# Kernel tuning notes

Hardware: AMD Instinct MI355X
Metric: run time of the kernel (lower is better)

The kernel has to match this reference:

```python
import jax, jax.numpy as jnp
import numpy as np

B, C, Np, D = 16, 64, 128, 128
HT = 4      # time heads
HS = 4      # space heads (GAT)
F = D       # GAT out_channels
DK = D // 2 # q/k proj dim
TOPK = 8
NEG = -1e30

def ln(x, g, b):
    m = x.mean(-1, keepdims=True)
    v = jnp.mean((x - m) ** 2, axis=-1, keepdims=True)
    return (x - m) / jnp.sqrt(v + 1e-5) * g + b

def setup_inputs() -> dict:
    key = jax.random.key(0)
    ks = jax.random.split(key, 16)
    w = lambda k, s: (jax.random.normal(k, s, jnp.float32) * 0.02)
    return dict(
        H_in=jax.random.normal(ks[0], (B, C, Np, D), jnp.float32),
        static_adj=jax.random.normal(ks[1], (C, C), jnp.float32) * 0.1,
        attn_in_w=w(ks[2], (3 * D, D)), attn_in_b=jnp.zeros((3 * D,), jnp.float32),
        attn_out_w=w(ks[3], (D, D)), attn_out_b=jnp.zeros((D,), jnp.float32),
        ln1_g=jnp.ones((D,), jnp.float32), ln1_b=jnp.zeros((D,), jnp.float32),
        ln2_g=jnp.ones((D,), jnp.float32), ln2_b=jnp.zeros((D,), jnp.float32),
        ff1_w=w(ks[4], (4 * D, D)), ff1_b=jnp.zeros((4 * D,), jnp.float32),
        ff2_w=w(ks[5], (D, 4 * D)), ff2_b=jnp.zeros((D,), jnp.float32),
        tnorm_g=jnp.ones((D,), jnp.float32), tnorm_b=jnp.zeros((D,), jnp.float32),
        q_w=w(ks[6], (DK, D)), q_b=jnp.zeros((DK,), jnp.float32),
        k_w=w(ks[7], (DK, D)), k_b=jnp.zeros((DK,), jnp.float32),
        gat_w=w(ks[8], (HS, F, D)),
        gat_att_src=w(ks[9], (HS, F)), gat_att_dst=w(ks[10], (HS, F)),
        gat_bias=jnp.zeros((D,), jnp.float32),
        snorm_g=jnp.ones((D,), jnp.float32), snorm_b=jnp.zeros((D,), jnp.float32),
    )

def _forward(H_in, static_adj, attn_in_w, attn_in_b, attn_out_w, attn_out_b,
             ln1_g, ln1_b, ln2_g, ln2_b, ff1_w, ff1_b, ff2_w, ff2_b,
             tnorm_g, tnorm_b, q_w, q_b, k_w, k_b,
             gat_w, gat_att_src, gat_att_dst, gat_bias, snorm_g, snorm_b):
    dh = D // HT
    # ---- temporal transformer encoder layer (norm_first) on [B*C, Np, D]
    x0 = H_in.reshape(B * C, Np, D)
    h = ln(x0, ln1_g, ln1_b)
    qkv = h @ attn_in_w.T + attn_in_b
    q, k, v = jnp.split(qkv, 3, axis=-1)
    q = q.reshape(-1, Np, HT, dh).transpose(0, 2, 1, 3)
    k = k.reshape(-1, Np, HT, dh).transpose(0, 2, 1, 3)
    v = v.reshape(-1, Np, HT, dh).transpose(0, 2, 1, 3)
    att = jax.nn.softmax(jnp.einsum('nhqd,nhkd->nhqk', q, k) / jnp.sqrt(jnp.float32(dh)), axis=-1)
    o = jnp.einsum('nhqk,nhkd->nhqd', att, v).transpose(0, 2, 1, 3).reshape(-1, Np, D)
    x = x0 + (o @ attn_out_w.T + attn_out_b)
    h2 = ln(x, ln2_g, ln2_b)
    x = x + jax.nn.relu(h2 @ ff1_w.T + ff1_b) @ ff2_w.T + ff2_b
    H_temp = ln(x0 + x, tnorm_g, tnorm_b).reshape(B, C, Np, D)
    # ---- dynamic adjacency from temporal summary
    Hs = H_temp.mean(axis=2)                              # [B,C,D]
    q2 = Hs @ q_w.T + q_b
    k2 = Hs @ k_w.T + k_b
    sim = jnp.einsum('bcd,bed->bce', q2, k2) * (DK ** -0.5)
    A = jnp.tanh(sim) + static_adj[None]                  # [B,C,C]
    # ---- top-k edge mask per sample (row r -> its top-k cols, no self loops)
    kk = max(1, min(TOPK, C - 1))
    idx = jax.lax.top_k(A, kk)[1]                         # [B,C,kk]
    mask = jnp.any(jax.nn.one_hot(idx, C, dtype=bool), axis=2)  # [B,C,C]
    mask = mask & (~jnp.eye(C, dtype=bool)) & (A != 0)
    # ---- dense masked GAT over all (B, Np) graphs; src=row, dst=col
    xh = jnp.einsum('bcpd,hfd->bphcf', H_temp, gat_w)     # [B,Np,HS,C,F]
    asrc = jnp.einsum('bphcf,hf->bphc', xh, gat_att_src)
    adst = jnp.einsum('bphcf,hf->bphc', xh, gat_att_dst)
    e = asrc[..., :, None] + adst[..., None, :]           # [B,Np,HS,src,dst]
    e = jnp.where(e > 0, e, 0.2 * e)                      # LeakyReLU(0.2)
    mb = mask[:, None, None, :, :]
    e = jnp.where(mb, e, NEG)
    e = e - e.max(axis=3, keepdims=True)                  # softmax over src per dst
    wgt = jnp.exp(e) * mb
    s = wgt.sum(axis=3, keepdims=True)
    a = wgt / jnp.where(s > 0, s, 1.0)
    out = jnp.einsum('bphst,bphsf->bphtf', a, xh).mean(axis=2) + gat_bias  # [B,Np,C,F]
    out = out.transpose(0, 2, 1, 3)                       # [B,C,Np,D]
    return ln(out + H_temp, snorm_g, snorm_b)

def reference(H_in, static_adj, attn_in_w, attn_in_b, attn_out_w, attn_out_b,
              ln1_g, ln1_b, ln2_g, ln2_b, ff1_w, ff1_b, ff2_w, ff2_b,
              tnorm_g, tnorm_b, q_w, q_b, k_w, k_b,
              gat_w, gat_att_src, gat_att_dst, gat_bias, snorm_g, snorm_b):
    return _forward(H_in, static_adj, attn_in_w, attn_in_b, attn_out_w, attn_out_b,
                    ln1_g, ln1_b, ln2_g, ln2_b, ff1_w, ff1_b, ff2_w, ff2_b,
                    tnorm_g, tnorm_b, q_w, q_b, k_w, k_b,
                    gat_w, gat_att_src, gat_att_dst, gat_bias, snorm_g, snorm_b)
```

## Files before the change

kernel.cpp:

```cpp
#include <hip/hip_runtime.h>
#include <cstdint>


typedef __attribute__((ext_vector_type(8)))  short bf16x8;
typedef __attribute__((ext_vector_type(16))) float f32x16;
#define MFMA32(a, b, c) __builtin_amdgcn_mfma_f32_32x32x16_bf16((a), (b), (c), 0, 0, 0)

__device__ __forceinline__ unsigned short f2bf(float f) {
    unsigned int u = __float_as_uint(f);
    u += 0x7fffu + ((u >> 16) & 1u);
    return (unsigned short)(u >> 16);
}
__device__ __forceinline__ float bf2f(unsigned short u) {
    return __uint_as_float(((unsigned int)u) << 16);
}

__device__ __forceinline__ bf16x8 lds_frag(const unsigned short* p) {
    union { bf16x8 v; ushort4 h[2]; } u;
    u.h[0] = *(const ushort4*)p;
    u.h[1] = *(const ushort4*)(p + 4);
    return u.v;
}
__device__ __forceinline__ bf16x8 gfrag(const unsigned short* p) {
    union { bf16x8 v; uint4 u; } t;
    t.u = *(const uint4*)p;
    return t.v;
}

__device__ __forceinline__ int rowmap(int r, int hl) { return (r & 3) + 8 * (r >> 2) + 4 * hl; }

__device__ __forceinline__ unsigned int pk2(float lo, float hi) {
    return (unsigned int)f2bf(lo) | ((unsigned int)f2bf(hi) << 16);
}

template<int B>
__device__ __forceinline__ bf16x8 pack_frag(const f32x16& p) {
    unsigned int a0 = pk2(p[B + 0], p[B + 1]);
    unsigned int a1 = pk2(p[B + 2], p[B + 3]);
    unsigned int b0 = pk2(p[B + 4], p[B + 5]);
    unsigned int b1 = pk2(p[B + 6], p[B + 7]);
    asm("v_permlane32_swap_b32 %0, %1" : "+v"(b0), "+v"(a0));
    asm("v_permlane32_swap_b32 %0, %1" : "+v"(b1), "+v"(a1));
    union { bf16x8 v; unsigned int w[4]; } u;
    u.w[0] = a0; u.w[1] = a1; u.w[2] = b0; u.w[3] = b1;
    return u.v;
}

__global__ void wconv_kernel(const float* __restrict__ wqkv, const float* __restrict__ wout,
                             const float* __restrict__ w1, const float* __restrict__ w2,
                             const float* __restrict__ gw,
                             unsigned short* __restrict__ dst) {
    int i = blockIdx.x * 256 + threadIdx.x;
    float v;
    if (i < 49152)       v = wqkv[i];
    else if (i < 65536)  v = wout[i - 49152];
    else if (i < 131072) v = w1[i - 65536];
    else if (i < 196608) v = w2[i - 131072];
    else                 v = gw[i - 196608];
    dst[i] = f2bf(v);
}

__global__ void wa_kernel(const float* __restrict__ gw, const float* __restrict__ asw,
                          const float* __restrict__ adw,
                          float* __restrict__ waS, float* __restrict__ waD) {
    int t = blockIdx.x * 256 + threadIdx.x;
    int h = t >> 8, d = (t >> 1) & 127, which = t & 1;
    const float* av = which ? adw : asw;
    float s = 0.f;
    for (int f = 0; f < 128; f++) s += av[h * 128 + f] * gw[(h * 128 + f) * 128 + d];
    (which ? waD : waS)[h * 128 + d] = s;
}

#define QKV_STAGE(H, KBB, VTB) do {                                              \
    f32x16 accq, acck, accv;                                                     \
    _Pragma("unroll") for (int r = 0; r < 16; r++)                               \
        accq[r] = bqkv[(H) * 32 + rowmap(r, hl)];                                \
    float bk_ = bqkv[128 + (H) * 32 + l31];                                      \
    float bv_ = bqkv[256 + (H) * 32 + l31];                                      \
    _Pragma("unroll") for (int r = 0; r < 16; r++) { acck[r] = bk_; accv[r] = bv_; } \
    const unsigned short* wq_ = wqkv_b + ((H) * 32 + l31) * 128 + hl * 8;        \
    const unsigned short* wk_ = wqkv_b + (128 + (H) * 32 + l31) * 128 + hl * 8;  \
    const unsigned short* wv_ = wqkv_b + (256 + (H) * 32 + l31) * 128 + hl * 8;  \
    _Pragma("unroll") for (int k0 = 0; k0 < 128; k0 += 16) {                     \
        bf16x8 a_ = lds_frag(&RA[myrow][k0 + hl * 8]);                           \
        accq = MFMA32(gfrag(wq_ + k0), a_, accq);   \
        acck = MFMA32(a_, gfrag(wk_ + k0), acck);                                \
        accv = MFMA32(a_, gfrag(wv_ + k0), accv);                                \
    }                                                                            \
    _Pragma("unroll") for (int r = 0; r < 16; r++) {                             \
        int tok_ = wv * 32 + rowmap(r, hl);                                      \
        KBB[tok_][l31] = f2bf(acck[r]);                                          \
        VTB[l31][tok_] = f2bf(accv[r]);                                          \
    }                                                                            \
    qf0_ = pack_frag<0>(accq);                                                   \
    qf1_ = pack_frag<8>(accq);                                                   \
} while (0)

#define ATTN_PHASE(H, KBB, VTB, NEXTQKV) do {                                    \
    f32x16 sacc[4];                                                              \
    _Pragma("unroll") for (int t = 0; t < 4; t++)                                \
    _Pragma("unroll") for (int r = 0; r < 16; r++) sacc[t][r] = 0.f;             \
    _Pragma("unroll") for (int t = 0; t < 4; t++) {                              \
        bf16x8 ka0 = lds_frag(&KBB[t * 32 + l31][hl * 8]);                       \
        sacc[t] = MFMA32(ka0, qf0_, sacc[t]);                                    \
        bf16x8 ka1 = lds_frag(&KBB[t * 32 + l31][16 + hl * 8]);                  \
        sacc[t] = MFMA32(ka1, qf1_, sacc[t]);                                    \
    }                                                                            \
    NEXTQKV;                                                                     \
    const float scale_ = 0.17677669529663687f;                   \
    float m0 = -1e30f;                                                           \
    _Pragma("unroll") for (int t = 0; t < 4; t++)                                \
    _Pragma("unroll") for (int r = 0; r < 16; r++) m0 = fmaxf(m0, sacc[t][r]);   \
    m0 = fmaxf(m0, __shfl_xor(m0, 32));                                          \
    float ssum = 0.f;                                                            \
    _Pragma("unroll") for (int t = 0; t < 4; t++)                                \
    _Pragma("unroll") for (int r = 0; r < 16; r++) {                             \
        float e_ = __expf(scale_ * (sacc[t][r] - m0));                           \
        sacc[t][r] = e_; ssum += e_;                                             \
    }                                                                            \
    ssum += __shfl_xor(ssum, 32);                                                \
    float rinv_ = 1.f / ssum;                                                    \
    _Pragma("unroll") for (int t = 0; t < 4; t++)                                \
    _Pragma("unroll") for (int r = 0; r < 16; r++) sacc[t][r] *= rinv_;          \
    f32x16 oacc;                                                                 \
    _Pragma("unroll") for (int r = 0; r < 16; r++) oacc[r] = 0.f;                \
    _Pragma("unroll") for (int t = 0; t < 4; t++) {                              \
        bf16x8 pf0 = pack_frag<0>(sacc[t]);                                      \
        bf16x8 v0_ = lds_frag(&VTB[l31][t * 32 + hl * 8]);                       \
        oacc = MFMA32(pf0, v0_, oacc);                                           \
        bf16x8 pf1 = pack_frag<8>(sacc[t]);                                      \
        bf16x8 v1_ = lds_frag(&VTB[l31][t * 32 + 16 + hl * 8]);                  \
        oacc = MFMA32(pf1, v1_, oacc);                                           \
    }                                                                            \
    _Pragma("unroll") for (int j = 0; j < 8; j++)                                \
        opk[H][j] = pk2(oacc[2*j], oacc[2*j+1]);                                 \
} while (0)

__global__ __launch_bounds__(256, 2)
void temporal_kernel(const float* __restrict__ Hin,
                     const unsigned short* __restrict__ wqkv_b, const float* __restrict__ bqkv,
                     const unsigned short* __restrict__ wout_b, const float* __restrict__ bout,
                     const float* __restrict__ g1, const float* __restrict__ b1,
                     const float* __restrict__ g2, const float* __restrict__ b2,
                     const unsigned short* __restrict__ w1_b, const float* __restrict__ bf1,
                     const unsigned short* __restrict__ w2_b, const float* __restrict__ bf2,
                     const float* __restrict__ tg, const float* __restrict__ tb,
                     float* __restrict__ Htemp, float* __restrict__ Hs) {
    __shared__ unsigned short RA[128][132];
    __shared__ double RBd[4416];
    unsigned short (*kb0)[36]  = (unsigned short(*)[36])RBd;
    unsigned short (*vT0)[132] = (unsigned short(*)[132])((char*)RBd + 9216);
    unsigned short (*kb1)[36]  = (unsigned short(*)[36])((char*)RBd + 17664);
    unsigned short (*vT1)[132] = (unsigned short(*)[132])((char*)RBd + 26880);
    unsigned short (*rscr)[32][36] = (unsigned short(*)[32][36])RBd;
    float (*hsred)[128] = (float(*)[128])((char*)RBd + 9216);

    const int n = blockIdx.x;
    const int tid = threadIdx.x;
    const int lane = tid & 63;
    const int wv = tid >> 6;
    const int hl = lane >> 5;
    const int l31 = lane & 31;
    const int myrow = wv * 32 + l31;

    {
        int row = tid >> 1, hf = tid & 1;
        const float* src = Hin + ((long)n * 128 + row) * 128 + hf * 64;
        float xv[64];
        float s = 0.f, qs = 0.f;
#pragma unroll
        for (int i = 0; i < 64; i += 4) {
            float4 t = *(const float4*)(src + i);
            xv[i] = t.x; xv[i+1] = t.y; xv[i+2] = t.z; xv[i+3] = t.w;
        }
#pragma unroll
        for (int i = 0; i < 64; i++) { s += xv[i]; qs += xv[i] * xv[i]; }
        s += __shfl_xor(s, 1); qs += __shfl_xor(qs, 1);
        float mu = s * 0.0078125f;
        float rs = rsqrtf(fmaxf(qs * 0.0078125f - mu * mu, 0.f) + 1e-5f);
#pragma unroll
        for (int i = 0; i < 64; i++) {
            int d = hf * 64 + i;
            RA[row][d] = f2bf((xv[i] - mu) * rs * g1[d] + b1[d]);
        }
    }

    unsigned int opk[4][8];
    bf16x8 qf0_, qf1_;

    QKV_STAGE(0, kb0, vT0);
    __syncthreads();
    ATTN_PHASE(0, kb0, vT0, QKV_STAGE(1, kb1, vT1));
    __syncthreads();
    ATTN_PHASE(1, kb1, vT1, QKV_STAGE(2, kb0, vT0));
    __syncthreads();
    ATTN_PHASE(2, kb0, vT0, QKV_STAGE(3, kb1, vT1));
    __syncthreads();
    ATTN_PHASE(3, kb1, vT1, (void)0);

#pragma unroll
    for (int h = 0; h < 4; h++)
#pragma unroll
        for (int j = 0; j < 8; j++) {
            int tok0 = wv * 32 + rowmap(2*j,     hl);
            int tok1 = wv * 32 + rowmap(2*j + 1, hl);
            RA[tok0][h * 32 + l31] = (unsigned short)(opk[h][j] & 0xffffu);
            RA[tok1][h * 32 + l31] = (unsigned short)(opk[h][j] >> 16);
        }

    f32x16 acc[4];
#pragma unroll
    for (int t = 0; t < 4; t++) {
        float bo = bout[t * 32 + l31];
#pragma unroll
        for (int r = 0; r < 16; r++) {
            int tok = wv * 32 + rowmap(r, hl);
            acc[t][r] = Hin[((long)n * 128 + tok) * 128 + t * 32 + l31] + bo;
        }
    }
#pragma unroll
    for (int k0 = 0; k0 < 128; k0 += 16) {
        bf16x8 a = lds_frag(&RA[myrow][k0 + hl * 8]);
#pragma unroll
        for (int t = 0; t < 4; t++) {
            bf16x8 b = gfrag(wout_b + (t * 32 + l31) * 128 + k0 + hl * 8);
            acc[t] = MFMA32(a, b, acc[t]);
        }
    }

#pragma unroll
    for (int r = 0; r < 16; r++) {
        float s = acc[0][r] + acc[1][r] + acc[2][r] + acc[3][r];
#pragma unroll
        for (int d = 1; d < 32; d <<= 1) s += __shfl_xor(s, d);
        float mu = s * 0.0078125f;
        float q = 0.f;
#pragma unroll
        for (int t = 0; t < 4; t++) { float dv = acc[t][r] - mu; q += dv * dv; }
#pragma unroll
        for (int d = 1; d < 32; d <<= 1) q += __shfl_xor(q, d);
        float rs = rsqrtf(q * 0.0078125f + 1e-5f);
        int row = wv * 32 + rowmap(r, hl);
#pragma unroll
        for (int t = 0; t < 4; t++) {
            int col = t * 32 + l31;
            RA[row][col] = f2bf((acc[t][r] - mu) * rs * g2[col] + b2[col]);
        }
    }

#pragma unroll
    for (int t = 0; t < 4; t++) {
        float bv = bf2[t * 32 + l31];
#pragma unroll
        for (int r = 0; r < 16; r++) acc[t][r] += bv;
    }

    for (int j = 0; j < 4; j++) {
        f32x16 racc[4];
#pragma unroll
        for (int t = 0; t < 4; t++) {
            float bv = bf1[j * 128 + t * 32 + l31];
#pragma unroll
            for (int r = 0; r < 16; r++) racc[t][r] = bv;
        }
#pragma unroll
        for (int k0 = 0; k0 < 128; k0 += 16) {
            bf16x8 a = lds_frag(&RA[myrow][k0 + hl * 8]);
#pragma unroll
            for (int t = 0; t < 4; t++) {
                bf16x8 b = gfrag(w1_b + (j * 128 + t * 32 + l31) * 128 + k0 + hl * 8);
                racc[t] = MFMA32(a, b, racc[t]);
            }
        }
#pragma unroll
        for (int t = 0; t < 4; t++) {
#pragma unroll
            for (int r = 0; r < 16; r++)
                rscr[wv][rowmap(r, hl)][l31] = f2bf(fmaxf(racc[t][r], 0.f));
#pragma unroll
            for (int kk = 0; kk < 32; kk += 16) {
                bf16x8 a = lds_frag(&rscr[wv][l31][kk + hl * 8]);
#pragma unroll
                for (int tp = 0; tp < 4; tp++) {
                    bf16x8 b = gfrag(w2_b + (tp * 32 + l31) * 512 + j * 128 + t * 32 + kk + hl * 8);
                    acc[tp] = MFMA32(a, b, acc[tp]);
                }
            }
        }
    }

#pragma unroll
    for (int t = 0; t < 4; t++)
#pragma unroll
        for (int r = 0; r < 16; r++) {
            int tok = wv * 32 + rowmap(r, hl);
            acc[t][r] += Hin[((long)n * 128 + tok) * 128 + t * 32 + l31];
        }
    float* outf = Htemp + (long)n * 16384;
    float cs0 = 0.f, cs1 = 0.f, cs2 = 0.f, cs3 = 0.f;
#pragma unroll
    for (int r = 0; r < 16; r++) {
        float s = acc[0][r] + acc[1][r] + acc[2][r] + acc[3][r];
#pragma unroll
        for (int d = 1; d < 32; d <<= 1) s += __shfl_xor(s, d);
        float mu = s * 0.0078125f;
        float q = 0.f;
#pragma unroll
        for (int t = 0; t < 4; t++) { float dv = acc[t][r] - mu; q += dv * dv; }
#pragma unroll
        for (int d = 1; d < 32; d <<= 1) q += __shfl_xor(q, d);
        float rs = rsqrtf(q * 0.0078125f + 1e-5f);
        int tok = wv * 32 + rowmap(r, hl);
        {
            float v = (acc[0][r] - mu) * rs * tg[0 * 32 + l31] + tb[0 * 32 + l31];
            outf[tok * 128 + 0 * 32 + l31] = v;  cs0 += v;
        }
        {
            float v = (acc[1][r] - mu) * rs * tg[1 * 32 + l31] + tb[1 * 32 + l31];
            outf[tok * 128 + 1 * 32 + l31] = v;  cs1 += v;
        }
        {
            float v = (acc[2][r] - mu) * rs * tg[2 * 32 + l31] + tb[2 * 32 + l31];
            outf[tok * 128 + 2 * 32 + l31] = v;  cs2 += v;
        }
        {
            float v = (acc[3][r] - mu) * rs * tg[3 * 32 + l31] + tb[3 * 32 + l31];
            outf[tok * 128 + 3 * 32 + l31] = v;  cs3 += v;
        }
    }
    cs0 += __shfl_xor(cs0, 32); cs1 += __shfl_xor(cs1, 32);
    cs2 += __shfl_xor(cs2, 32); cs3 += __shfl_xor(cs3, 32);
    if (hl == 0) {
        hsred[wv][0 * 32 + l31] = cs0;
        hsred[wv][1 * 32 + l31] = cs1;
        hsred[wv][2 * 32 + l31] = cs2;
        hsred[wv][3 * 32 + l31] = cs3;
    }
    __syncthreads();
    if (tid < 128)
        Hs[(long)n * 128 + tid] =
            (hsred[0][tid] + hsred[1][tid] + hsred[2][tid] + hsred[3][tid]) * 0.0078125f;
}

__global__ __launch_bounds__(256)
void graph_kernel(const float* __restrict__ Hs,
                  const float* __restrict__ qw, const float* __restrict__ qb,
                  const float* __restrict__ kw, const float* __restrict__ kb,
                  const float* __restrict__ adj, unsigned long long* __restrict__ masks) {
    __shared__ float q2l[64][65];
    __shared__ float k2l[64][65];
    __shared__ float am[64][65];
    int b = blockIdx.x;
    int tid = threadIdx.x;
    {
        int r = tid & 127, jh = tid >> 7;
        int row = r & 63;
        const float* wmat = (r < 64) ? qw : kw;
        const float* bvec = (r < 64) ? qb : kb;
        const float* src = Hs + (long)(b * 64 + row) * 128;
        for (int jj = 0; jj < 32; jj++) {
            int j = jh * 32 + jj;
            const float* wrow = wmat + (long)j * 128;
            float s0 = 0.f, s1 = 0.f, s2 = 0.f, s3 = 0.f;
#pragma unroll
            for (int d = 0; d < 128; d += 4) {
                s0 += src[d] * wrow[d];     s1 += src[d+1] * wrow[d+1];
                s2 += src[d+2] * wrow[d+2]; s3 += src[d+3] * wrow[d+3];
            }
            float val = ((s0 + s1) + (s2 + s3)) + bvec[j];
            if (r < 64) q2l[row][j] = val; else k2l[row][j] = val;
        }
    }
    __syncthreads();
    {
        int c = tid & 63, eq = tid >> 6;
        for (int ee = 0; ee < 16; ee++) {
            int e = eq * 16 + ee;
            float s0 = 0.f, s1 = 0.f, s2 = 0.f, s3 = 0.f;
#pragma unroll
            for (int j = 0; j < 64; j += 4) {
                s0 += q2l[c][j]   * k2l[e][j];
                s1 += q2l[c][j+1] * k2l[e][j+1];
                s2 += q2l[c][j+2] * k2l[e][j+2];
                s3 += q2l[c][j+3] * k2l[e][j+3];
            }
            float sim = ((s0 + s1) + (s2 + s3)) * 0.125f;
            am[c][e] = tanhf(sim) + adj[c * 64 + e];
        }
    }
    __syncthreads();
    if (tid < 64) {
        int c = tid;
        unsigned long long sel = 0ull;
        for (int it = 0; it < 8; it++) {
            float best = -1e38f; int bi = 0;
            for (int e = 0; e < 64; e++) {
                float v = am[c][e];
                bool ok = (((sel >> e) & 1ull) == 0ull) && (v > best);
                best = ok ? v : best;
                bi = ok ? e : bi;
            }
            sel |= (1ull << bi);
        }
        sel &= ~(1ull << c);
        for (int e = 0; e < 64; e++)
            if (am[c][e] == 0.f) sel &= ~(1ull << e);
        masks[b * 64 + c] = sel;
    }
}

#define XH_STAGE(H, XT) do {                                                     \
    f32x16 a0_, a1_;                                                             \
    _Pragma("unroll") for (int r = 0; r < 16; r++) { a0_[r] = 0.f; a1_[r] = 0.f; } \
    const unsigned short* gwh_ = gwb + (H) * 16384;                              \
    _Pragma("unroll") for (int k0 = 0; k0 < 128; k0 += 16) {                     \
        bf16x8 af_ = lds_frag(&Htb[rs + l31][k0 + hl * 8]);                      \
        bf16x8 b0_ = gfrag(gwh_ + (cs + l31) * 128 + k0 + hl * 8);               \
        bf16x8 b1_ = gfrag(gwh_ + (cs + 32 + l31) * 128 + k0 + hl * 8);          \
        a0_ = MFMA32(af_, b0_, a0_);                                             \
        a1_ = MFMA32(af_, b1_, a1_);                                             \
    }                                                                            \
    _Pragma("unroll") for (int g = 0; g < 4; g++) {                              \
        ushort4 u0_, u1_;                                                        \
        u0_.x = f2bf(a0_[4*g]);   u0_.y = f2bf(a0_[4*g+1]);                      \
        u0_.z = f2bf(a0_[4*g+2]); u0_.w = f2bf(a0_[4*g+3]);                      \
        u1_.x = f2bf(a1_[4*g]);   u1_.y = f2bf(a1_[4*g+1]);                      \
        u1_.z = f2bf(a1_[4*g+2]); u1_.w = f2bf(a1_[4*g+3]);                      \
        int so_ = rs + 4 * hl + 8 * g;                                           \
        *(ushort4*)&XT[cs + l31][so_]      = u0_;                                \
        *(ushort4*)&XT[cs + 32 + l31][so_] = u1_;                                \
    }                                                                            \
} while (0)

#define PV_PHASE(H, XT, NEXTXH) do {                                             \
    float adv_ = adstF[H][rs + l31];                    \
    float ev_[4][8];                                                             \
    float M_ = -1e30f;                                                           \
    _Pragma("unroll") for (int q = 0; q < 4; q++)                                \
    _Pragma("unroll") for (int j = 0; j < 8; j++) {                              \
        int s_ = q * 16 + hl * 8 + j;                                            \
        float e_ = asrcF[H][s_] + adv_;                                          \
        e_ = (e_ > 0.f) ? e_ : 0.2f * e_;                                        \
        ev_[q][j] = e_;                                                          \
        if ((mt >> s_) & 1ull) M_ = fmaxf(M_, e_);                               \
    }                                                                            \
    M_ = fmaxf(M_, __shfl_xor(M_, 32));                                          \
    float sm_ = 0.f;                                                             \
    _Pragma("unroll") for (int q = 0; q < 4; q++)                                \
    _Pragma("unroll") for (int j = 0; j < 8; j++) {                              \
        int s_ = q * 16 + hl * 8 + j;                                            \
        float w_ = ((mt >> s_) & 1ull) ? __expf(ev_[q][j] - M_) : 0.f;           \
        ev_[q][j] = w_; sm_ += w_;                                               \
    }                                                                            \
    sm_ += __shfl_xor(sm_, 32);                                                  \
    float rinv_ = (sm_ > 0.f) ? 1.f / sm_ : 0.f;                                 \
    NEXTXH;                                                                      \
    _Pragma("unroll") for (int q = 0; q < 4; q++) {                              \
        union { bf16x8 v; unsigned int w[4]; } uu_;                              \
        uu_.w[0] = pk2(ev_[q][0] * rinv_, ev_[q][1] * rinv_);                    \
        uu_.w[1] = pk2(ev_[q][2] * rinv_, ev_[q][3] * rinv_);                    \
        uu_.w[2] = pk2(ev_[q][4] * rinv_, ev_[q][5] * rinv_);                    \
        uu_.w[3] = pk2(ev_[q][6] * rinv_, ev_[q][7] * rinv_);                    \
        bf16x8 af_ = uu_.v;                                                      \
        oacc0 = MFMA32(af_, lds_frag(&XT[cs + l31][q * 16 + hl * 8]), oacc0);    \
        oacc1 = MFMA32(af_, lds_frag(&XT[cs + 32 + l31][q * 16 + hl * 8]), oacc1); \
    }                                                                            \
} while (0)

__global__ __launch_bounds__(256, 2)
void gat_kernel(float* __restrict__ Htemp,
                const unsigned short* __restrict__ gwb,
                const float* __restrict__ waS, const float* __restrict__ waD,
                const float* __restrict__ gbias,
                const unsigned long long* __restrict__ masks,
                const float* __restrict__ sg, const float* __restrict__ sb) {
    __shared__ unsigned short Htb[64][132];
    __shared__ double xbuf0[2176];
    __shared__ double xbuf1[2176];
    __shared__ float asrcF[4][64], adstF[4][64];
    __shared__ float pr0[2][64], pr1[2][64];
    __shared__ unsigned long long mk[64];
    __shared__ unsigned long long mTT[64];

    unsigned short (*xhT0)[68] = (unsigned short(*)[68])xbuf0;
    unsigned short (*xhT1)[68] = (unsigned short(*)[68])xbuf1;
    float (*part)[8][64]       = (float(*)[8][64])xbuf0;

    const int bp = blockIdx.x;
    const int b = bp >> 7, p = bp & 127;
    const int tid = threadIdx.x;
    const int lane = tid & 63, wv = tid >> 6;
    const int hl = lane >> 5, l31 = lane & 31;
    const int rs = (wv & 1) * 32;
    const int cs = (wv >> 1) * 64;

    {
        int c = tid >> 2, qq = tid & 3;
        const float* src = Htemp + ((long)(b * 64 + c) * 128 + p) * 128 + qq * 32;
#pragma unroll
        for (int k = 0; k < 8; k++) {
            float4 t4 = *(const float4*)(src + 4 * k);
            ushort4 u; u.x = f2bf(t4.x); u.y = f2bf(t4.y); u.z = f2bf(t4.z); u.w = f2bf(t4.w);
            *(ushort4*)&Htb[c][qq * 32 + 4 * k] = u;
        }
    }
    if (tid < 64) mk[tid] = masks[b * 64 + tid];
    __syncthreads();

    {
        int s = lane, q = wv;
        float acc[8];
#pragma unroll
        for (int m = 0; m < 8; m++) acc[m] = 0.f;
        const unsigned int* hp = (const unsigned int*)&Htb[s][q * 32];
#pragma unroll
        for (int d2 = 0; d2 < 16; d2++) {
            unsigned int u = hp[d2];
            float f0 = __uint_as_float(u << 16);
            float f1 = __uint_as_float(u & 0xffff0000u);
            int d = q * 32 + 2 * d2;
#pragma unroll
            for (int h = 0; h < 4; h++) {
                acc[2*h]   += f0 * waS[h * 128 + d] + f1 * waS[h * 128 + d + 1];
                acc[2*h+1] += f0 * waD[h * 128 + d] + f1 * waD[h * 128 + d + 1];
            }
        }
#pragma unroll
        for (int m = 0; m < 8; m++) part[q][m][s] = acc[m];
    }
    __syncthreads();
    for (int o = tid; o < 512; o += 256) {
        int h = o >> 7, rem = o & 127, which = rem >> 6, s = rem & 63;
        int m = h * 2 + which;
        float v = part[0][m][s] + part[1][m][s] + part[2][m][s] + part[3][m][s];
        if (which == 0) asrcF[h][s] = v; else adstF[h][s] = v;
    }
    if (tid < 64) {
        unsigned long long m = 0ull;
        for (int s = 0; s < 64; s++)
            m |= ((mk[s] >> tid) & 1ull) << s;
        mTT[tid] = m;
    }
    __syncthreads();

    const unsigned long long mt = mTT[rs + l31];

    f32x16 oacc0, oacc1;
#pragma unroll
    for (int r = 0; r < 16; r++) { oacc0[r] = 0.f; oacc1[r] = 0.f; }

    XH_STAGE(0, xhT0);
    __syncthreads();
    PV_PHASE(0, xhT0, XH_STAGE(1, xhT1));
    __syncthreads();
    PV_PHASE(1, xhT1, XH_STAGE(2, xhT0));
    __syncthreads();
    PV_PHASE(2, xhT0, XH_STAGE(3, xhT1));
    __syncthreads();
    PV_PHASE(3, xhT1, (void)0);

    float gb0 = gbias[cs + l31], gb1 = gbias[cs + 32 + l31];
    float v0[16], v1[16];
#pragma unroll
    for (int r = 0; r < 16; r++) {
        int c = rs + rowmap(r, hl);
        v0[r] = oacc0[r] * 0.25f + gb0 + bf2f(Htb[c][cs + l31]);
        v1[r] = oacc1[r] * 0.25f + gb1 + bf2f(Htb[c][cs + 32 + l31]);
    }
#pragma unroll
    for (int r = 0; r < 16; r++) {
        float s = v0[r] + v1[r];
        float q = v0[r] * v0[r] + v1[r] * v1[r];
#pragma unroll
        for (int d = 1; d < 32; d <<= 1) { s += __shfl_xor(s, d); q += __shfl_xor(q, d); }
        if (l31 == 0) {
            int c = rs + rowmap(r, hl);
            pr0[wv >> 1][c] = s;
            pr1[wv >> 1][c] = q;
        }
    }
    __syncthreads();
    float sgv0 = sg[cs + l31], sbv0 = sb[cs + l31];
    float sgv1 = sg[cs + 32 + l31], sbv1 = sb[cs + 32 + l31];
#pragma unroll
    for (int r = 0; r < 16; r++) {
        int c = rs + rowmap(r, hl);
        float sum = pr0[0][c] + pr0[1][c];
        float sq  = pr1[0][c] + pr1[1][c];
        float mu = sum * 0.0078125f;
        float var = sq * 0.0078125f - mu * mu;
        float rsd = rsqrtf(fmaxf(var, 0.f) + 1e-5f);
        float* orow = Htemp + ((long)(b * 64 + c) * 128 + p) * 128;
        orow[cs + l31]      = (v0[r] - mu) * rsd * sgv0 + sbv0;
        orow[cs + 32 + l31] = (v1[r] - mu) * rsd * sgv1 + sbv1;
    }
}

extern "C" void kernel_launch(void* const* d_in, const int* in_sizes, int n_in,
                              void* d_out, int out_size, void* d_ws, size_t ws_size,
                              hipStream_t stream) {
    const float* Hin        = (const float*)d_in[0];
    const float* static_adj = (const float*)d_in[1];
    const float* attn_in_w  = (const float*)d_in[2];
    const float* attn_in_b  = (const float*)d_in[3];
    const float* attn_out_w = (const float*)d_in[4];
    const float* attn_out_b = (const float*)d_in[5];
    const float* ln1_g      = (const float*)d_in[6];
    const float* ln1_b      = (const float*)d_in[7];
    const float* ln2_g      = (const float*)d_in[8];
    const float* ln2_b      = (const float*)d_in[9];
    const float* ff1_w      = (const float*)d_in[10];
    const float* ff1_b      = (const float*)d_in[11];
    const float* ff2_w      = (const float*)d_in[12];
    const float* ff2_b      = (const float*)d_in[13];
    const float* tnorm_g    = (const float*)d_in[14];
    const float* tnorm_b    = (const float*)d_in[15];
    const float* q_w        = (const float*)d_in[16];
    const float* q_b        = (const float*)d_in[17];
    const float* k_w        = (const float*)d_in[18];
    const float* k_b        = (const float*)d_in[19];
    const float* gat_w      = (const float*)d_in[20];
    const float* gat_att_src= (const float*)d_in[21];
    const float* gat_att_dst= (const float*)d_in[22];
    const float* gat_bias   = (const float*)d_in[23];
    const float* snorm_g    = (const float*)d_in[24];
    const float* snorm_b    = (const float*)d_in[25];

    float* out = (float*)d_out;
    char* ws = (char*)d_ws;
    unsigned short* wb = (unsigned short*)ws;
    const unsigned short* wqkv_b = wb;
    const unsigned short* wout_b = wb + 49152;
    const unsigned short* w1_b   = wb + 65536;
    const unsigned short* w2_b   = wb + 131072;
    const unsigned short* gw_b   = wb + 196608;
    unsigned long long* masks = (unsigned long long*)(ws + 524288);
    float* Hs  = (float*)(ws + 532480);
    float* waS = (float*)(ws + 1056768);
    float* waD = (float*)(ws + 1058816);

    hipLaunchKernelGGL(wconv_kernel, dim3(1024), dim3(256), 0, stream,
                       attn_in_w, attn_out_w, ff1_w, ff2_w, gat_w, wb);
    hipLaunchKernelGGL(wa_kernel, dim3(4), dim3(256), 0, stream,
                       gat_w, gat_att_src, gat_att_dst, waS, waD);
    hipLaunchKernelGGL(temporal_kernel, dim3(1024), dim3(256), 0, stream,
                       Hin, wqkv_b, attn_in_b, wout_b, attn_out_b,
                       ln1_g, ln1_b, ln2_g, ln2_b,
                       w1_b, ff1_b, w2_b, ff2_b, tnorm_g, tnorm_b, out, Hs);
    hipLaunchKernelGGL(graph_kernel, dim3(16), dim3(256), 0, stream,
                       Hs, q_w, q_b, k_w, k_b, static_adj, masks);
    hipLaunchKernelGGL(gat_kernel, dim3(2048), dim3(256), 0, stream,
                       out, gw_b, waS, waD, gat_bias,
                       masks, snorm_g, snorm_b);
}
```

Baseline: 567.1 us.

## Stage temporal output as transposed bf16 for GAT, merge prep kernels, raise GAT occupancy

The temporal kernel now writes its layer-norm output as bf16 in a [B,Np,C,D] layout to a workspace buffer instead of fp32 Htemp. The GAT kernel then reads contiguous bf16 rows rather than gathering strided fp32 values. The GAT kernel also drops the double-buffered xh staging in favour of a single buffer in a loop, and raises launch bounds to 4 blocks per CU. The two weight-prep kernels are merged into one launch. This cuts global traffic and launch overhead, but loses the overlap of staging with the PV phase and depends on the workspace being large enough. When the workspace is too small it falls back to the fp32 path.

Result: faster. 532.1 us (median of 3 runs) (-6.2%).

```diff
diff --git a/kernel.cpp b/kernel.cpp
--- a/kernel.cpp
+++ b/kernel.cpp
@@ -46,29 +46,29 @@
     return u.v;
 }
 
-__global__ void wconv_kernel(const float* __restrict__ wqkv, const float* __restrict__ wout,
-                             const float* __restrict__ w1, const float* __restrict__ w2,
-                             const float* __restrict__ gw,
-                             unsigned short* __restrict__ dst) {
-    int i = blockIdx.x * 256 + threadIdx.x;
-    float v;
-    if (i < 49152)       v = wqkv[i];
-    else if (i < 65536)  v = wout[i - 49152];
-    else if (i < 131072) v = w1[i - 65536];
-    else if (i < 196608) v = w2[i - 131072];
-    else                 v = gw[i - 196608];
-    dst[i] = f2bf(v);
-}
-
-__global__ void wa_kernel(const float* __restrict__ gw, const float* __restrict__ asw,
-                          const float* __restrict__ adw,
-                          float* __restrict__ waS, float* __restrict__ waD) {
-    int t = blockIdx.x * 256 + threadIdx.x;
-    int h = t >> 8, d = (t >> 1) & 127, which = t & 1;
-    const float* av = which ? adw : asw;
-    float s = 0.f;
-    for (int f = 0; f < 128; f++) s += av[h * 128 + f] * gw[(h * 128 + f) * 128 + d];
-    (which ? waD : waS)[h * 128 + d] = s;
+__global__ void prep_kernel(const float* __restrict__ wqkv, const float* __restrict__ wout,
+                            const float* __restrict__ w1, const float* __restrict__ w2,
+                            const float* __restrict__ gw,
+                            const float* __restrict__ asw, const float* __restrict__ adw,
+                            unsigned short* __restrict__ dst,
+                            float* __restrict__ waS, float* __restrict__ waD) {
+    if (blockIdx.x < 1024) {
+        int i = blockIdx.x * 256 + threadIdx.x;
+        float v;
+        if (i < 49152)       v = wqkv[i];
+        else if (i < 65536)  v = wout[i - 49152];
+        else if (i < 131072) v = w1[i - 65536];
+        else if (i < 196608) v = w2[i - 131072];
+        else                 v = gw[i - 196608];
+        dst[i] = f2bf(v);
+    } else {
+        int t = (blockIdx.x - 1024) * 256 + threadIdx.x;
+        int h = t >> 8, d = (t >> 1) & 127, which = t & 1;
+        const float* av = which ? adw : asw;
+        float s = 0.f;
+        for (int f = 0; f < 128; f++) s += av[h * 128 + f] * gw[(h * 128 + f) * 128 + d];
+        (which ? waD : waS)[h * 128 + d] = s;
+    }
 }
 
 #define QKV_STAGE(H, KBB, VTB) do {                                              \
@@ -136,6 +136,7 @@
         opk[H][j] = pk2(oacc[2*j], oacc[2*j+1]);                                 \
 } while (0)
 
+template<int BF16>
 __global__ __launch_bounds__(256, 2)
 void temporal_kernel(const float* __restrict__ Hin,
                      const unsigned short* __restrict__ wqkv_b, const float* __restrict__ bqkv,
@@ -145,7 +146,8 @@
                      const unsigned short* __restrict__ w1_b, const float* __restrict__ bf1,
                      const unsigned short* __restrict__ w2_b, const float* __restrict__ bf2,
                      const float* __restrict__ tg, const float* __restrict__ tb,
-                     float* __restrict__ Htemp, float* __restrict__ Hs) {
+                     float* __restrict__ Htemp, float* __restrict__ Hs,
+                     unsigned short* __restrict__ hbt) {
     __shared__ unsigned short RA[128][132];
     __shared__ double RBd[4416];
     unsigned short (*kb0)[36]  = (unsigned short(*)[36])RBd;
@@ -296,6 +298,7 @@
             int tok = wv * 32 + rowmap(r, hl);
             acc[t][r] += Hin[((long)n * 128 + tok) * 128 + t * 32 + l31];
         }
+    const int bb = n >> 6, cc = n & 63;
     float* outf = Htemp + (long)n * 16384;
     float cs0 = 0.f, cs1 = 0.f, cs2 = 0.f, cs3 = 0.f;
 #pragma unroll
@@ -311,21 +314,22 @@
         for (int d = 1; d < 32; d <<= 1) q += __shfl_xor(q, d);
         float rs = rsqrtf(q * 0.0078125f + 1e-5f);
         int tok = wv * 32 + rowmap(r, hl);
-        {
-            float v = (acc[0][r] - mu) * rs * tg[0 * 32 + l31] + tb[0 * 32 + l31];
-            outf[tok * 128 + 0 * 32 + l31] = v;  cs0 += v;
-        }
-        {
-            float v = (acc[1][r] - mu) * rs * tg[1 * 32 + l31] + tb[1 * 32 + l31];
-            outf[tok * 128 + 1 * 32 + l31] = v;  cs1 += v;
-        }
-        {
-            float v = (acc[2][r] - mu) * rs * tg[2 * 32 + l31] + tb[2 * 32 + l31];
-            outf[tok * 128 + 2 * 32 + l31] = v;  cs2 += v;
-        }
-        {
-            float v = (acc[3][r] - mu) * rs * tg[3 * 32 + l31] + tb[3 * 32 + l31];
-            outf[tok * 128 + 3 * 32 + l31] = v;  cs3 += v;
+        float v0 = (acc[0][r] - mu) * rs * tg[0 * 32 + l31] + tb[0 * 32 + l31];
+        float v1 = (acc[1][r] - mu) * rs * tg[1 * 32 + l31] + tb[1 * 32 + l31];
+        float v2 = (acc[2][r] - mu) * rs * tg[2 * 32 + l31] + tb[2 * 32 + l31];
+        float v3 = (acc[3][r] - mu) * rs * tg[3 * 32 + l31] + tb[3 * 32 + l31];
+        cs0 += v0; cs1 += v1; cs2 += v2; cs3 += v3;
+        if constexpr (BF16) {
+            unsigned short* ob = hbt + ((long)(bb * 128 + tok) * 64 + cc) * 128 + l31;
+            ob[0]  = f2bf(v0);
+            ob[32] = f2bf(v1);
+            ob[64] = f2bf(v2);
+            ob[96] = f2bf(v3);
+        } else {
+            outf[tok * 128 + 0 * 32 + l31] = v0;
+            outf[tok * 128 + 1 * 32 + l31] = v1;
+            outf[tok * 128 + 2 * 32 + l31] = v2;
+            outf[tok * 128 + 3 * 32 + l31] = v3;
         }
     }
     cs0 += __shfl_xor(cs0, 32); cs1 += __shfl_xor(cs1, 32);
@@ -432,7 +436,7 @@
     }                                                                            \
 } while (0)
 
-#define PV_PHASE(H, XT, NEXTXH) do {                                             \
+#define PV_PHASE(H, XT) do {                                                     \
     float adv_ = adstF[H][rs + l31];                    \
     float ev_[4][8];                                                             \
     float M_ = -1e30f;                                                           \
@@ -454,7 +458,6 @@
     }                                                                            \
     sm_ += __shfl_xor(sm_, 32);                                                  \
     float rinv_ = (sm_ > 0.f) ? 1.f / sm_ : 0.f;                                 \
-    NEXTXH;                                                                      \
     _Pragma("unroll") for (int q = 0; q < 4; q++) {                              \
         union { bf16x8 v; unsigned int w[4]; } uu_;                              \
         uu_.w[0] = pk2(ev_[q][0] * rinv_, ev_[q][1] * rinv_);                    \
@@ -467,24 +470,24 @@
     }                                                                            \
 } while (0)
 
-__global__ __launch_bounds__(256, 2)
+template<int BF16>
+__global__ __launch_bounds__(256, 4)
 void gat_kernel(float* __restrict__ Htemp,
+                const unsigned short* __restrict__ hbt,
                 const unsigned short* __restrict__ gwb,
                 const float* __restrict__ waS, const float* __restrict__ waD,
                 const float* __restrict__ gbias,
                 const unsigned long long* __restrict__ masks,
                 const float* __restrict__ sg, const float* __restrict__ sb) {
     __shared__ unsigned short Htb[64][132];
-    __shared__ double xbuf0[2176];
-    __shared__ double xbuf1[2176];
+    __shared__ double xbuf[2176];
     __shared__ float asrcF[4][64], adstF[4][64];
     __shared__ float pr0[2][64], pr1[2][64];
     __shared__ unsigned long long mk[64];
     __shared__ unsigned long long mTT[64];
 
-    unsigned short (*xhT0)[68] = (unsigned short(*)[68])xbuf0;
-    unsigned short (*xhT1)[68] = (unsigned short(*)[68])xbuf1;
-    float (*part)[8][64]       = (float(*)[8][64])xbuf0;
+    unsigned short (*xhT)[68] = (unsigned short(*)[68])xbuf;
+    float (*part)[8][64]      = (float(*)[8][64])xbuf;
 
     const int bp = blockIdx.x;
     const int b = bp >> 7, p = bp & 127;
@@ -494,7 +497,13 @@
     const int rs = (wv & 1) * 32;
     const int cs = (wv >> 1) * 64;
 
-    {
+    if constexpr (BF16) {
+        int c = tid >> 2, qq = tid & 3;
+        const unsigned short* src = hbt + ((long)(b * 128 + p) * 64 + c) * 128 + qq * 32;
+#pragma unroll
+        for (int m = 0; m < 8; m++)
+            *(ushort4*)&Htb[c][qq * 32 + 4 * m] = *(const ushort4*)(src + 4 * m);
+    } else {
         int c = tid >> 2, qq = tid & 3;
         const float* src = Htemp + ((long)(b * 64 + c) * 128 + p) * 128 + qq * 32;
 #pragma unroll
@@ -549,15 +558,12 @@
 #pragma unroll
     for (int r = 0; r < 16; r++) { oacc0[r] = 0.f; oacc1[r] = 0.f; }
 
-    XH_STAGE(0, xhT0);
-    __syncthreads();
-    PV_PHASE(0, xhT0, XH_STAGE(1, xhT1));
-    __syncthreads();
-    PV_PHASE(1, xhT1, XH_STAGE(2, xhT0));
-    __syncthreads();
-    PV_PHASE(2, xhT0, XH_STAGE(3, xhT1));
-    __syncthreads();
-    PV_PHASE(3, xhT1, (void)0);
+    for (int h = 0; h < 4; h++) {
+        XH_STAGE(h, xhT);
+        __syncthreads();
+        PV_PHASE(h, xhT);
+        __syncthreads();
+    }
 
     float gb0 = gbias[cs + l31], gb1 = gbias[cs + 32 + l31];
     float v0[16], v1[16];
@@ -638,18 +644,31 @@
     float* Hs  = (float*)(ws + 532480);
     float* waS = (float*)(ws + 1056768);
     float* waD = (float*)(ws + 1058816);
-
-    hipLaunchKernelGGL(wconv_kernel, dim3(1024), dim3(256), 0, stream,
-                       attn_in_w, attn_out_w, ff1_w, ff2_w, gat_w, wb);
-    hipLaunchKernelGGL(wa_kernel, dim3(4), dim3(256), 0, stream,
-                       gat_w, gat_att_src, gat_att_dst, waS, waD);
-    hipLaunchKernelGGL(temporal_kernel, dim3(1024), dim3(256), 0, stream,
-                       Hin, wqkv_b, attn_in_b, wout_b, attn_out_b,
-                       ln1_g, ln1_b, ln2_g, ln2_b,
-                       w1_b, ff1_b, w2_b, ff2_b, tnorm_g, tnorm_b, out, Hs);
-    hipLaunchKernelGGL(graph_kernel, dim3(16), dim3(256), 0, stream,
-                       Hs, q_w, q_b, k_w, k_b, static_adj, masks);
-    hipLaunchKernelGGL(gat_kernel, dim3(2048), dim3(256), 0, stream,
-                       out, gw_b, waS, waD, gat_bias,
-                       masks, snorm_g, snorm_b);
-}
+    unsigned short* hbt = (unsigned short*)(ws + 1060864);
+    const bool big_ws = ws_size >= (size_t)(1060864 + 33554432);
+
+    hipLaunchKernelGGL(prep_kernel, dim3(1028), dim3(256), 0, stream,
+                       attn_in_w, attn_out_w, ff1_w, ff2_w, gat_w,
+                       gat_att_src, gat_att_dst, wb, waS, waD);
+    if (big_ws) {
+        hipLaunchKernelGGL((temporal_kernel<1>), dim3(1024), dim3(256), 0, stream,
+                           Hin, wqkv_b, attn_in_b, wout_b, attn_out_b,
+                           ln1_g, ln1_b, ln2_g, ln2_b,
+                           w1_b, ff1_b, w2_b, ff2_b, tnorm_g, tnorm_b, out, Hs, hbt);
+        hipLaunchKernelGGL(graph_kernel, dim3(16), dim3(256), 0, stream,
+                           Hs, q_w, q_b, k_w, k_b, static_adj, masks);
+        hipLaunchKernelGGL((gat_kernel<1>), dim3(2048), dim3(256), 0, stream,
+                           out, hbt, gw_b, waS, waD, gat_bias,
+                           masks, snorm_g, snorm_b);
+    } else {
+        hipLaunchKernelGGL((temporal_kernel<0>), dim3(1024), dim3(256), 0, stream,
+                           Hin, wqkv_b, attn_in_b, wout_b, attn_out_b,
+                           ln1_g, ln1_b, ln2_g, ln2_b,
+                           w1_b, ff1_b, w2_b, ff2_b, tnorm_g, tnorm_b, out, Hs, hbt);
+        hipLaunchKernelGGL(graph_kernel, dim3(16), dim3(256), 0, stream,
+                           Hs, q_w, q_b, k_w, k_b, static_adj, masks);
+        hipLaunchKernelGGL((gat_kernel<0>), dim3(2048), dim3(256), 0, stream,
+                           out, hbt, gw_b, waS, waD, gat_bias,
+                           masks, snorm_g, snorm_b);
+    }
+}
```
